# Kernel tuning notes

Measured on AMD Instinct MI355X. Metric: run time of the kernel, lower is better.

## Reference

```python
import jax, jax.numpy as jnp
import numpy as np

B, L, D, H, NB = 32, 200, 512, 8, 2
HD = D // H
EPS = 1e-8


def _ln(x, g, b):
    m = x.mean(-1, keepdims=True)
    v = ((x - m) ** 2).mean(-1, keepdims=True)
    return (x - m) / jnp.sqrt(v + EPS) * g + b


def setup_inputs() -> dict:
    key = jax.random.key(0)
    ks = jax.random.split(key, 12)
    w = lambda k, shape: (jax.random.normal(k, shape, jnp.float32) * 0.02)
    return {
        "x": jax.random.normal(ks[0], (B, L, D), jnp.float32),
        "timeline_mask": jnp.zeros((B, L), dtype=bool),  # True = padded
        "ln1_g": jnp.ones((NB, D), jnp.float32), "ln1_b": jnp.zeros((NB, D), jnp.float32),
        "Wq": w(ks[1], (NB, D, D)), "bq": jnp.zeros((NB, D), jnp.float32),
        "Wk": w(ks[2], (NB, D, D)), "bk": jnp.zeros((NB, D), jnp.float32),
        "Wv": w(ks[3], (NB, D, D)), "bv": jnp.zeros((NB, D), jnp.float32),
        "Wo": w(ks[4], (NB, D, D)), "bo": jnp.zeros((NB, D), jnp.float32),
        "ln2_g": jnp.ones((NB, D), jnp.float32), "ln2_b": jnp.zeros((NB, D), jnp.float32),
        "W1": w(ks[5], (NB, D, D)), "b1": jnp.zeros((NB, D), jnp.float32),
        "W2": w(ks[6], (NB, D, D)), "b2": jnp.zeros((NB, D), jnp.float32),
        "lnf_g": jnp.ones((D,), jnp.float32), "lnf_b": jnp.zeros((D,), jnp.float32),
    }


def reference(x, timeline_mask, ln1_g, ln1_b, Wq, bq, Wk, bk, Wv, bv, Wo, bo,
              ln2_g, ln2_b, W1, b1, W2, b2, lnf_g, lnf_b):
    valid = (~timeline_mask)[..., None].astype(x.dtype)  # [B,L,1]
    # causal additive bias [L,L]: 0 on/below diag, -inf above
    causal = jnp.where(jnp.tril(jnp.ones((L, L), dtype=bool)), 0.0, -jnp.inf).astype(x.dtype)
    scale = 1.0 / (HD ** 0.5)
    q = x * valid  # dropout = identity (eval)
    for i in range(NB):
        Qn = _ln(q, ln1_g[i], ln1_b[i])  # pre-attn LayerNorm (query side)
        qh = (Qn @ Wq[i] + bq[i]).reshape(B, L, H, HD)
        kh = (q @ Wk[i] + bk[i]).reshape(B, L, H, HD)
        vh = (q @ Wv[i] + bv[i]).reshape(B, L, H, HD)
        scores = jnp.einsum('bqhd,bkhd->bhqk', qh, kh) * scale + causal
        attn = jax.nn.softmax(scores, axis=-1)
        ctx = jnp.einsum('bhqk,bkhd->bqhd', attn, vh).reshape(B, L, D)
        q = ctx @ Wo[i] + bo[i] + Qn          # residual to normed Q (as in source)
        q = _ln(q, ln2_g[i], ln2_b[i])        # forward layernorm
        h = jax.nn.relu(q @ W1[i] + b1[i]) @ W2[i] + b2[i]  # 1x1 convs == per-token MLP
        q = (q + h) * valid                   # PWFF residual, then timeline mask
    return _ln(q, lnf_g, lnf_b)
```

## Files before the change

kernel.cpp:

```cpp
#include <hip/hip_runtime.h>

typedef unsigned short u16;
typedef __bf16 bfloat;
typedef bfloat bf16x8 __attribute__((ext_vector_type(8)));
typedef float f32x4 __attribute__((ext_vector_type(4)));
typedef u16 v8u16 __attribute__((ext_vector_type(8)));
typedef u16 v4u16 __attribute__((ext_vector_type(4)));

#define B_ 32
#define L_ 200
#define D_ 512
#define H_ 8
#define HD_ 64
#define M_ (B_*L_)

__device__ __forceinline__ float bf2f(u16 u) {
  union { float f; unsigned int i; } v; v.i = ((unsigned int)u) << 16; return v.f;
}
__device__ __forceinline__ u16 f2bf(float f) {
  union { float f; unsigned int i; } v; v.f = f;
  unsigned int i = v.i;
  return (u16)((i + 0x7FFFu + ((i >> 16) & 1u)) >> 16);
}

__device__ __forceinline__ void gload16(const void* g, void* l) {
  __builtin_amdgcn_global_load_lds(
      (const __attribute__((address_space(1))) void*)g,
      (__attribute__((address_space(3))) void*)l,
      16, 0, 0);
}

struct TPtrs { const float* s[12]; };

__global__ __launch_bounds__(256) void prep_kernel(
    const float* __restrict__ x, const unsigned char* __restrict__ mask,
    u16* __restrict__ qb, TPtrs tp, u16* __restrict__ dst)
{
  __shared__ float T[64][65];
  int bid = blockIdx.x;
  int t = threadIdx.x;
  if (bid < 1600) {
    size_t i = (size_t)bid * 256 + t;
    size_t base = i * 8;
    int tok = (int)(base >> 9);
    float valid = mask[tok] ? 0.f : 1.f;
    float4 v0 = *(const float4*)(x + base);
    float4 v1 = *(const float4*)(x + base + 4);
    v8u16 ob;
    ob[0]=f2bf(v0.x*valid); ob[1]=f2bf(v0.y*valid); ob[2]=f2bf(v0.z*valid); ob[3]=f2bf(v0.w*valid);
    ob[4]=f2bf(v1.x*valid); ob[5]=f2bf(v1.y*valid); ob[6]=f2bf(v1.z*valid); ob[7]=f2bf(v1.w*valid);
    *(v8u16*)(qb + base) = ob;
  } else {
    int wb   = bid - 1600;
    int mat  = wb >> 6;
    int tile = wb & 63;
    int tr = tile >> 3, tc = tile & 7;
    const float* src = tp.s[mat];
    #pragma unroll
    for (int i = 0; i < 4; i++) {
      int idx = t + i * 256;
      int row = idx >> 4, c4 = idx & 15;
      float4 v = *(const float4*)(src + (size_t)(tr * 64 + row) * 512 + tc * 64 + c4 * 4);
      T[row][c4 * 4 + 0] = v.x; T[row][c4 * 4 + 1] = v.y;
      T[row][c4 * 4 + 2] = v.z; T[row][c4 * 4 + 3] = v.w;
    }
    __syncthreads();
    u16* d = dst + (size_t)mat * 262144;
    #pragma unroll
    for (int i = 0; i < 2; i++) {
      int idx = t + i * 256;
      int row = idx >> 3, c8 = idx & 7;
      v8u16 v;
      #pragma unroll
      for (int j = 0; j < 8; j++) v[j] = f2bf(T[c8 * 8 + j][row]);
      *(v8u16*)(d + (size_t)(tc * 64 + row) * 512 + tr * 64 + c8 * 8) = v;
    }
  }
}

template<bool OUTF32>
__global__ __launch_bounds__(256) void ln_kernel(
    const u16* __restrict__ in, const float* __restrict__ g, const float* __restrict__ b,
    u16* __restrict__ outb, float* __restrict__ outf)
{
  int row  = blockIdx.x * 4 + (threadIdx.x >> 6);
  int lane = threadIdx.x & 63;
  size_t base = (size_t)row * 512 + lane * 8;
  v8u16 xv = *(const v8u16*)(in + base);
  float xs[8];
  #pragma unroll
  for (int j = 0; j < 8; j++) xs[j] = bf2f(xv[j]);
  float s = 0.f, q = 0.f;
  #pragma unroll
  for (int j = 0; j < 8; j++) { s += xs[j]; q += xs[j] * xs[j]; }
  #pragma unroll
  for (int off = 1; off < 64; off <<= 1) { s += __shfl_xor(s, off); q += __shfl_xor(q, off); }
  float mean = s * (1.f / 512.f);
  float var  = fmaxf(q * (1.f / 512.f) - mean * mean, 0.f);
  float rstd = rsqrtf(var + 1e-8f);
  float4 g0 = *(const float4*)(g + lane * 8);
  float4 g1 = *(const float4*)(g + lane * 8 + 4);
  float4 b0 = *(const float4*)(b + lane * 8);
  float4 b1 = *(const float4*)(b + lane * 8 + 4);
  float gv[8] = {g0.x,g0.y,g0.z,g0.w,g1.x,g1.y,g1.z,g1.w};
  float bv[8] = {b0.x,b0.y,b0.z,b0.w,b1.x,b1.y,b1.z,b1.w};
  if (OUTF32) {
    float of[8];
    #pragma unroll
    for (int j = 0; j < 8; j++) of[j] = (xs[j] - mean) * rstd * gv[j] + bv[j];
    *(float4*)(outf + base)     = make_float4(of[0], of[1], of[2], of[3]);
    *(float4*)(outf + base + 4) = make_float4(of[4], of[5], of[6], of[7]);
  } else {
    v8u16 ob;
    #pragma unroll
    for (int j = 0; j < 8; j++) ob[j] = f2bf((xs[j] - mean) * rstd * gv[j] + bv[j]);
    *(v8u16*)(outb + base) = ob;
  }
}

template<bool RELU, bool HAS_RES, bool MASK>
__device__ __forceinline__ void gemm_body(
    const u16* __restrict__ A, const u16* __restrict__ Wt, const float* __restrict__ bias,
    const u16* __restrict__ res, const unsigned char* __restrict__ mask,
    u16* __restrict__ outb, int m0, int n0, u16* As, u16* Bs)
{
  int tid = threadIdx.x, wid = tid >> 6, lane = tid & 63;
  int wr = wid >> 1, wc = wid & 1;
  int l15 = lane & 15, hi = lane >> 4;
  int sr8 = lane >> 3;
  int gsw = (lane & 7) ^ sr8;

  f32x4 acc[2][4] = {};

  for (int s = 0; s < 8; s++) {
    int kk = s * 64;
    #pragma unroll
    for (int i = 0; i < 2; i++) {
      int rbase = i * 32 + wid * 8;
      gload16(A + (size_t)(m0 + rbase + sr8) * 512 + kk + gsw * 8, (char*)As + rbase * 128);
    }
    #pragma unroll
    for (int j = 0; j < 4; j++) {
      int rbase = j * 32 + wid * 8;
      gload16(Wt + (size_t)(n0 + rbase + sr8) * 512 + kk + gsw * 8, (char*)Bs + rbase * 128);
    }
    __syncthreads();
    #pragma unroll
    for (int ksub = 0; ksub < 2; ksub++) {
      int ga = ksub * 4 + hi;
      bf16x8 af[2], bfr[4];
      #pragma unroll
      for (int mi = 0; mi < 2; mi++) {
        int ra = wr * 32 + mi * 16 + l15;
        af[mi] = *(const bf16x8*)(As + ra * 64 + ((ga ^ (ra & 7)) * 8));
      }
      #pragma unroll
      for (int ni = 0; ni < 4; ni++) {
        int rb = wc * 64 + ni * 16 + l15;
        bfr[ni] = *(const bf16x8*)(Bs + rb * 64 + ((ga ^ (rb & 7)) * 8));
      }
      #pragma unroll
      for (int mi = 0; mi < 2; mi++)
        #pragma unroll
        for (int ni = 0; ni < 4; ni++)
          acc[mi][ni] = __builtin_amdgcn_mfma_f32_16x16x32_bf16(af[mi], bfr[ni], acc[mi][ni], 0, 0, 0);
    }
    __syncthreads();
  }

  #pragma unroll
  for (int ni = 0; ni < 4; ni++) {
    int gc = n0 + wc * 64 + ni * 16 + l15;
    float bvv = bias[gc];
    #pragma unroll
    for (int mi = 0; mi < 2; mi++) {
      int grb = m0 + wr * 32 + mi * 16 + hi * 4;
      #pragma unroll
      for (int r = 0; r < 4; r++) {
        int gr = grb + r;
        float v = acc[mi][ni][r] + bvv;
        if (HAS_RES) v += bf2f(res[(size_t)gr * 512 + gc]);
        if (RELU) v = fmaxf(v, 0.f);
        if (MASK) v = mask[gr] ? 0.f : v;
        outb[(size_t)gr * 512 + gc] = f2bf(v);
      }
    }
  }
}

template<bool RELU, bool HAS_RES, bool MASK>
__global__ __launch_bounds__(256) void gemm_one(
    const u16* __restrict__ A, const u16* __restrict__ Wt, const float* __restrict__ bias,
    const u16* __restrict__ res, const unsigned char* __restrict__ mask,
    u16* __restrict__ outb)
{
  __shared__ u16 As[64 * 64];
  __shared__ u16 Bs[128 * 64];
  int bid = blockIdx.x;
  int m0 = (bid >> 2) * 64, n0 = (bid & 3) * 128;
  gemm_body<RELU, HAS_RES, MASK>(A, Wt, bias, res, mask, outb, m0, n0, As, Bs);
}

__global__ __launch_bounds__(256) void gemm_qkv(
    const u16* __restrict__ Aq, const u16* __restrict__ Akv,
    const u16* __restrict__ Wtq, const u16* __restrict__ Wtk, const u16* __restrict__ Wtv,
    const float* __restrict__ bq, const float* __restrict__ bk, const float* __restrict__ bv,
    u16* __restrict__ outq, u16* __restrict__ outk, u16* __restrict__ outv)
{
  __shared__ u16 As[64 * 64];
  __shared__ u16 Bs[128 * 64];
  int bid = blockIdx.x;
  int mat = bid / 400;
  int r = bid - mat * 400;
  int m0 = (r >> 2) * 64, n0 = (r & 3) * 128;
  const u16*   A    = (mat == 0) ? Aq  : Akv;
  const u16*   Wt   = (mat == 0) ? Wtq : ((mat == 1) ? Wtk : Wtv);
  const float* bias = (mat == 0) ? bq  : ((mat == 1) ? bk  : bv);
  u16*         outb = (mat == 0) ? outq : ((mat == 1) ? outk : outv);
  gemm_body<false, false, false>(A, Wt, bias, nullptr, nullptr, outb, m0, n0, As, Bs);
}

__global__ __launch_bounds__(256) void transposeV(const u16* __restrict__ Vh, u16* __restrict__ Vt) {
  int bh = blockIdx.x, b = bh >> 3, h = bh & 7;
  __shared__ u16 T[64 * 224];
  int tid = threadIdx.x;
  v8u16 z = {0,0,0,0,0,0,0,0};
  for (int idx = tid; idx < 64 * 224 / 8; idx += 256) *(v8u16*)(T + idx * 8) = z;
  __syncthreads();
  const u16* src = Vh + (size_t)(b * L_) * D_ + h * HD_;
  for (int idx = tid; idx < 200 * 8; idx += 256) {
    int l = idx >> 3, c = idx & 7;
    v8u16 v = *(const v8u16*)(src + (size_t)l * D_ + c * 8);
    #pragma unroll
    for (int j = 0; j < 8; j++) T[(c * 8 + j) * 224 + l] = v[j];
  }
  __syncthreads();
  u16* dst = Vt + (size_t)bh * 64 * 224;
  for (int idx = tid; idx < 64 * 224 / 8; idx += 256) *(v8u16*)(dst + idx * 8) = *(const v8u16*)(T + idx * 8);
}

__global__ __launch_bounds__(256) void attn_kernel(
    const u16* __restrict__ Qh, const u16* __restrict__ Kh,
    const u16* __restrict__ Vt, u16* __restrict__ ctx)
{
  __shared__ u16 Kl[208 * 64];
  __shared__ u16 Pl[4 * 16 * 224];
  int bh = blockIdx.x, b = bh >> 3, h = bh & 7;
  int tid = threadIdx.x;

  const u16* Kg = Kh + (size_t)(b * L_) * D_ + h * HD_;
  for (int idx = tid; idx < 208 * 8; idx += 256) {
    int row = idx >> 3, c = idx & 7;
    v8u16 v = {0,0,0,0,0,0,0,0};
    if (row < L_) v = *(const v8u16*)(Kg + (size_t)row * D_ + c * 8);
    *(v8u16*)(Kl + row * 64 + c * 8) = v;
  }
  __syncthreads();

  int wid = tid >> 6, lane = tid & 63;
  int l15 = lane & 15, hi = lane >> 4;
  u16* Pw = Pl + wid * 16 * 224;
  const u16* Vg = Vt + (size_t)bh * 64 * 224;
  {
    v4u16 z4 = {0,0,0,0};
    *(v4u16*)(Pw + l15 * 224 + 208 + hi * 4) = z4;
  }

  for (int t = wid; t < 13; t += 4) {
    int q0 = t * 16;
    int qrow = q0 + l15; if (qrow > L_ - 1) qrow = L_ - 1;
    const u16* Qg = Qh + (size_t)(b * L_ + qrow) * D_ + h * HD_ + hi * 8;
    bf16x8 aq0 = *(const bf16x8*)(Qg);
    bf16x8 aq1 = *(const bf16x8*)(Qg + 32);

    f32x4 sv[13];
    float m0[4];
    #pragma unroll
    for (int r = 0; r < 4; r++) m0[r] = -3.0e38f;

    #pragma unroll
    for (int kt = 0; kt < 13; kt++) {
      const u16* kp = Kl + (kt * 16 + l15) * 64 + hi * 8;
      bf16x8 bk0 = *(const bf16x8*)(kp);
      bf16x8 bk1 = *(const bf16x8*)(kp + 32);
      f32x4 a = {0.f, 0.f, 0.f, 0.f};
      a = __builtin_amdgcn_mfma_f32_16x16x32_bf16(aq0, bk0, a, 0, 0, 0);
      a = __builtin_amdgcn_mfma_f32_16x16x32_bf16(aq1, bk1, a, 0, 0, 0);
      #pragma unroll
      for (int r = 0; r < 4; r++) {
        int qr = q0 + hi * 4 + r;
        int kc = kt * 16 + l15;
        float val = (kc <= qr && qr < L_) ? a[r] * 0.125f : -3.0e38f;
        sv[kt][r] = val;
        m0[r] = fmaxf(m0[r], val);
      }
    }
    #pragma unroll
    for (int r = 0; r < 4; r++) {
      #pragma unroll
      for (int off = 1; off < 16; off <<= 1)
        m0[r] = fmaxf(m0[r], __shfl_xor(m0[r], off));
      if (m0[r] < -1e37f) m0[r] = 0.f;
    }
    float sum[4] = {0.f, 0.f, 0.f, 0.f};
    #pragma unroll
    for (int kt = 0; kt < 13; kt++) {
      #pragma unroll
      for (int r = 0; r < 4; r++) {
        float p = __expf(sv[kt][r] - m0[r]);
        sv[kt][r] = p;
        sum[r] += p;
      }
    }
    #pragma unroll
    for (int r = 0; r < 4; r++) {
      #pragma unroll
      for (int off = 1; off < 16; off <<= 1) sum[r] += __shfl_xor(sum[r], off);
    }
    float inv[4];
    #pragma unroll
    for (int r = 0; r < 4; r++) inv[r] = sum[r] > 0.f ? 1.f / sum[r] : 0.f;

    #pragma unroll
    for (int kt = 0; kt < 13; kt++) {
      #pragma unroll
      for (int r = 0; r < 4; r++)
        Pw[(hi * 4 + r) * 224 + kt * 16 + l15] = f2bf(sv[kt][r]);
    }
    asm volatile("" ::: "memory");

    #pragma unroll
    for (int nt = 0; nt < 4; nt++) {
      f32x4 a = {0.f, 0.f, 0.f, 0.f};
      #pragma unroll
      for (int ks = 0; ks < 7; ks++) {
        bf16x8 ap = *(const bf16x8*)(Pw + l15 * 224 + ks * 32 + hi * 8);
        bf16x8 bv = *(const bf16x8*)(Vg + (nt * 16 + l15) * 224 + ks * 32 + hi * 8);
        a = __builtin_amdgcn_mfma_f32_16x16x32_bf16(ap, bv, a, 0, 0, 0);
      }
      #pragma unroll
      for (int r = 0; r < 4; r++) {
        int qr = q0 + hi * 4 + r;
        if (qr < L_) ctx[(size_t)(b * L_ + qr) * D_ + h * HD_ + nt * 16 + l15] = f2bf(a[r] * inv[r]);
      }
    }
    asm volatile("" ::: "memory");
  }
}

extern "C" void kernel_launch(void* const* d_in, const int* in_sizes, int n_in,
                              void* d_out, int out_size, void* d_ws, size_t ws_size,
                              hipStream_t stream)
{
  (void)in_sizes; (void)n_in; (void)out_size; (void)ws_size;
  const float* x    = (const float*)d_in[0];
  const unsigned char* mask = (const unsigned char*)d_in[1];
  const float* ln1g = (const float*)d_in[2];
  const float* ln1b = (const float*)d_in[3];
  const float* Wq   = (const float*)d_in[4];
  const float* bq   = (const float*)d_in[5];
  const float* Wk   = (const float*)d_in[6];
  const float* bk   = (const float*)d_in[7];
  const float* Wv   = (const float*)d_in[8];
  const float* bv   = (const float*)d_in[9];
  const float* Wo   = (const float*)d_in[10];
  const float* bo   = (const float*)d_in[11];
  const float* ln2g = (const float*)d_in[12];
  const float* ln2b = (const float*)d_in[13];
  const float* W1   = (const float*)d_in[14];
  const float* b1   = (const float*)d_in[15];
  const float* W2   = (const float*)d_in[16];
  const float* b2   = (const float*)d_in[17];
  const float* lnfg = (const float*)d_in[18];
  const float* lnfb = (const float*)d_in[19];

  char* ws = (char*)d_ws;
  u16* Wt  = (u16*)(ws);
  u16* qb  = (u16*)(ws +  6291456);
  u16* Qn  = (u16*)(ws + 12845056);
  u16* qh  = (u16*)(ws + 19398656);
  u16* kh  = (u16*)(ws + 25952256);
  u16* vh  = (u16*)(ws + 32505856);
  u16* Vtb = (u16*)(ws + 39059456);

  TPtrs tp;
  tp.s[0] = Wq; tp.s[1] = Wq + 262144;
  tp.s[2] = Wk; tp.s[3] = Wk + 262144;
  tp.s[4] = Wv; tp.s[5] = Wv + 262144;
  tp.s[6] = Wo; tp.s[7] = Wo + 262144;
  tp.s[8] = W1; tp.s[9] = W1 + 262144;
  tp.s[10] = W2; tp.s[11] = W2 + 262144;

  prep_kernel<<<dim3(2368), dim3(256), 0, stream>>>(x, mask, qb, tp, Wt);

  for (int i = 0; i < 2; i++) {
    const u16* Wtq = Wt + (size_t)(0 + i) * 262144;
    const u16* Wtk = Wt + (size_t)(2 + i) * 262144;
    const u16* Wtv = Wt + (size_t)(4 + i) * 262144;
    const u16* Wto = Wt + (size_t)(6 + i) * 262144;
    const u16* Wt1 = Wt + (size_t)(8 + i) * 262144;
    const u16* Wt2 = Wt + (size_t)(10 + i) * 262144;

    ln_kernel<false><<<dim3(1600), dim3(256), 0, stream>>>(qb, ln1g + i * 512, ln1b + i * 512, Qn, nullptr);
    gemm_qkv<<<dim3(1200), dim3(256), 0, stream>>>(Qn, qb, Wtq, Wtk, Wtv,
                                                   bq + i * 512, bk + i * 512, bv + i * 512,
                                                   qh, kh, vh);
    transposeV<<<dim3(256), dim3(256), 0, stream>>>(vh, Vtb);
    attn_kernel<<<dim3(256), dim3(256), 0, stream>>>(qh, kh, Vtb, vh);
    gemm_one<false,true,false><<<dim3(400), dim3(256), 0, stream>>>(vh, Wto, bo + i * 512, Qn, nullptr, qb);
    ln_kernel<false><<<dim3(1600), dim3(256), 0, stream>>>(qb, ln2g + i * 512, ln2b + i * 512, Qn, nullptr);
    gemm_one<true,false,false><<<dim3(400), dim3(256), 0, stream>>>(Qn, Wt1, b1 + i * 512, nullptr, nullptr, qh);
    gemm_one<false,true,true><<<dim3(400), dim3(256), 0, stream>>>(qh, Wt2, b2 + i * 512, Qn, mask, qb);
  }
  ln_kernel<true><<<dim3(1600), dim3(256), 0, stream>>>(qb, lnfg, lnfb, nullptr, (float*)d_out);
}
```

Before: 211.2 us.

## Double-buffer GEMM k-loop, fuse V transpose into QKV epilogue, skip causal tiles

The GEMM core now prefetches the next k-slice into a second LDS buffer while computing on the current one, using explicit vmcnt waits and raw barriers. The QKV GEMM writes V directly in the transposed per-head layout, so the separate transposeV kernel and its round trip are removed. Attention skips QK^T, exp and PV work for key tiles above the causal diagonal. A risk: the padded columns of the transposed V buffer are no longer zeroed, so garbage there could leak into the last PV tile.

```diff
diff --git a/kernel.cpp b/kernel.cpp
--- a/kernel.cpp
+++ b/kernel.cpp
@@ -118,11 +118,9 @@
   }
 }
 
-template<bool RELU, bool HAS_RES, bool MASK>
-__device__ __forceinline__ void gemm_body(
-    const u16* __restrict__ A, const u16* __restrict__ Wt, const float* __restrict__ bias,
-    const u16* __restrict__ res, const unsigned char* __restrict__ mask,
-    u16* __restrict__ outb, int m0, int n0, u16* As, u16* Bs)
+__device__ __forceinline__ void gemm_core(
+    const u16* __restrict__ A, const u16* __restrict__ Wt,
+    int m0, int n0, u16* As, u16* Bs, f32x4 (&acc)[2][4])
 {
   int tid = threadIdx.x, wid = tid >> 6, lane = tid & 63;
   int wr = wid >> 1, wc = wid & 1;
@@ -130,21 +128,34 @@
   int sr8 = lane >> 3;
   int gsw = (lane & 7) ^ sr8;
 
-  f32x4 acc[2][4] = {};
-
+#define STAGE(buf, kk) do { \
+    _Pragma("unroll") \
+    for (int i_ = 0; i_ < 2; i_++) { \
+      int rb_ = i_ * 32 + wid * 8; \
+      gload16(A + (size_t)(m0 + rb_ + sr8) * 512 + (kk) + gsw * 8, \
+              (char*)As + (buf) * 8192 + rb_ * 128); \
+    } \
+    _Pragma("unroll") \
+    for (int j_ = 0; j_ < 4; j_++) { \
+      int rb_ = j_ * 32 + wid * 8; \
+      gload16(Wt + (size_t)(n0 + rb_ + sr8) * 512 + (kk) + gsw * 8, \
+              (char*)Bs + (buf) * 16384 + rb_ * 128); \
+    } } while (0)
+
+  STAGE(0, 0);
+  #pragma unroll
   for (int s = 0; s < 8; s++) {
-    int kk = s * 64;
-    #pragma unroll
-    for (int i = 0; i < 2; i++) {
-      int rbase = i * 32 + wid * 8;
-      gload16(A + (size_t)(m0 + rbase + sr8) * 512 + kk + gsw * 8, (char*)As + rbase * 128);
-    }
-    #pragma unroll
-    for (int j = 0; j < 4; j++) {
-      int rbase = j * 32 + wid * 8;
-      gload16(Wt + (size_t)(n0 + rbase + sr8) * 512 + kk + gsw * 8, (char*)Bs + rbase * 128);
-    }
-    __syncthreads();
+    int cur = s & 1;
+    if (s < 7) {
+      STAGE(cur ^ 1, (s + 1) * 64);
+      asm volatile("s_waitcnt vmcnt(6)" ::: "memory");
+    } else {
+      asm volatile("s_waitcnt vmcnt(0)" ::: "memory");
+    }
+    __builtin_amdgcn_s_barrier();
+    __builtin_amdgcn_sched_barrier(0);
+    const u16* Asb = As + cur * 4096;
+    const u16* Bsb = Bs + cur * 8192;
     #pragma unroll
     for (int ksub = 0; ksub < 2; ksub++) {
       int ga = ksub * 4 + hi;
@@ -152,12 +163,12 @@
       #pragma unroll
       for (int mi = 0; mi < 2; mi++) {
         int ra = wr * 32 + mi * 16 + l15;
-        af[mi] = *(const bf16x8*)(As + ra * 64 + ((ga ^ (ra & 7)) * 8));
+        af[mi] = *(const bf16x8*)(Asb + ra * 64 + ((ga ^ (ra & 7)) * 8));
       }
       #pragma unroll
       for (int ni = 0; ni < 4; ni++) {
         int rb = wc * 64 + ni * 16 + l15;
-        bfr[ni] = *(const bf16x8*)(Bs + rb * 64 + ((ga ^ (rb & 7)) * 8));
+        bfr[ni] = *(const bf16x8*)(Bsb + rb * 64 + ((ga ^ (rb & 7)) * 8));
       }
       #pragma unroll
       for (int mi = 0; mi < 2; mi++)
@@ -165,9 +176,28 @@
         for (int ni = 0; ni < 4; ni++)
           acc[mi][ni] = __builtin_amdgcn_mfma_f32_16x16x32_bf16(af[mi], bfr[ni], acc[mi][ni], 0, 0, 0);
     }
-    __syncthreads();
-  }
-
+    __builtin_amdgcn_sched_barrier(0);
+    __builtin_amdgcn_s_barrier();
+  }
+#undef STAGE
+}
+
+template<bool RELU, bool HAS_RES, bool MASK>
+__global__ __launch_bounds__(256) void gemm_one(
+    const u16* __restrict__ A, const u16* __restrict__ Wt, const float* __restrict__ bias,
+    const u16* __restrict__ res, const unsigned char* __restrict__ mask,
+    u16* __restrict__ outb)
+{
+  __shared__ u16 As[2 * 64 * 64];
+  __shared__ u16 Bs[2 * 128 * 64];
+  int bid = blockIdx.x;
+  int m0 = (bid >> 2) * 64, n0 = (bid & 3) * 128;
+  f32x4 acc[2][4] = {};
+  gemm_core(A, Wt, m0, n0, As, Bs, acc);
+
+  int tid = threadIdx.x, wid = tid >> 6, lane = tid & 63;
+  int wr = wid >> 1, wc = wid & 1;
+  int l15 = lane & 15, hi = lane >> 4;
   #pragma unroll
   for (int ni = 0; ni < 4; ni++) {
     int gc = n0 + wc * 64 + ni * 16 + l15;
@@ -188,55 +218,61 @@
   }
 }
 
-template<bool RELU, bool HAS_RES, bool MASK>
-__global__ __launch_bounds__(256) void gemm_one(
-    const u16* __restrict__ A, const u16* __restrict__ Wt, const float* __restrict__ bias,
-    const u16* __restrict__ res, const unsigned char* __restrict__ mask,
-    u16* __restrict__ outb)
-{
-  __shared__ u16 As[64 * 64];
-  __shared__ u16 Bs[128 * 64];
-  int bid = blockIdx.x;
-  int m0 = (bid >> 2) * 64, n0 = (bid & 3) * 128;
-  gemm_body<RELU, HAS_RES, MASK>(A, Wt, bias, res, mask, outb, m0, n0, As, Bs);
-}
-
 __global__ __launch_bounds__(256) void gemm_qkv(
     const u16* __restrict__ Aq, const u16* __restrict__ Akv,
     const u16* __restrict__ Wtq, const u16* __restrict__ Wtk, const u16* __restrict__ Wtv,
     const float* __restrict__ bq, const float* __restrict__ bk, const float* __restrict__ bv,
-    u16* __restrict__ outq, u16* __restrict__ outk, u16* __restrict__ outv)
-{
-  __shared__ u16 As[64 * 64];
-  __shared__ u16 Bs[128 * 64];
+    u16* __restrict__ outq, u16* __restrict__ outk, u16* __restrict__ outvt)
+{
+  __shared__ u16 As[2 * 64 * 64];
+  __shared__ u16 Bs[2 * 128 * 64];
   int bid = blockIdx.x;
   int mat = bid / 400;
-  int r = bid - mat * 400;
-  int m0 = (r >> 2) * 64, n0 = (r & 3) * 128;
+  int rr = bid - mat * 400;
+  int m0 = (rr >> 2) * 64, n0 = (rr & 3) * 128;
   const u16*   A    = (mat == 0) ? Aq  : Akv;
   const u16*   Wt   = (mat == 0) ? Wtq : ((mat == 1) ? Wtk : Wtv);
   const float* bias = (mat == 0) ? bq  : ((mat == 1) ? bk  : bv);
-  u16*         outb = (mat == 0) ? outq : ((mat == 1) ? outk : outv);
-  gemm_body<false, false, false>(A, Wt, bias, nullptr, nullptr, outb, m0, n0, As, Bs);
-}
-
-__global__ __launch_bounds__(256) void transposeV(const u16* __restrict__ Vh, u16* __restrict__ Vt) {
-  int bh = blockIdx.x, b = bh >> 3, h = bh & 7;
-  __shared__ u16 T[64 * 224];
-  int tid = threadIdx.x;
-  v8u16 z = {0,0,0,0,0,0,0,0};
-  for (int idx = tid; idx < 64 * 224 / 8; idx += 256) *(v8u16*)(T + idx * 8) = z;
-  __syncthreads();
-  const u16* src = Vh + (size_t)(b * L_) * D_ + h * HD_;
-  for (int idx = tid; idx < 200 * 8; idx += 256) {
-    int l = idx >> 3, c = idx & 7;
-    v8u16 v = *(const v8u16*)(src + (size_t)l * D_ + c * 8);
-    #pragma unroll
-    for (int j = 0; j < 8; j++) T[(c * 8 + j) * 224 + l] = v[j];
-  }
-  __syncthreads();
-  u16* dst = Vt + (size_t)bh * 64 * 224;
-  for (int idx = tid; idx < 64 * 224 / 8; idx += 256) *(v8u16*)(dst + idx * 8) = *(const v8u16*)(T + idx * 8);
+  f32x4 acc[2][4] = {};
+  gemm_core(A, Wt, m0, n0, As, Bs, acc);
+
+  int tid = threadIdx.x, wid = tid >> 6, lane = tid & 63;
+  int wr = wid >> 1, wc = wid & 1;
+  int l15 = lane & 15, hi = lane >> 4;
+  if (mat == 2) {
+    #pragma unroll
+    for (int ni = 0; ni < 4; ni++) {
+      int gc = n0 + wc * 64 + ni * 16 + l15;
+      float bvv = bias[gc];
+      int h = gc >> 6, hd = gc & 63;
+      #pragma unroll
+      for (int mi = 0; mi < 2; mi++) {
+        int grb = m0 + wr * 32 + mi * 16 + hi * 4;
+        #pragma unroll
+        for (int r = 0; r < 4; r++) {
+          int gr = grb + r;
+          int b = gr / 200, l = gr - b * 200;
+          outvt[((size_t)(b * 8 + h) * 64 + hd) * 224 + l] = f2bf(acc[mi][ni][r] + bvv);
+        }
+      }
+    }
+  } else {
+    u16* outb = (mat == 0) ? outq : outk;
+    #pragma unroll
+    for (int ni = 0; ni < 4; ni++) {
+      int gc = n0 + wc * 64 + ni * 16 + l15;
+      float bvv = bias[gc];
+      #pragma unroll
+      for (int mi = 0; mi < 2; mi++) {
+        int grb = m0 + wr * 32 + mi * 16 + hi * 4;
+        #pragma unroll
+        for (int r = 0; r < 4; r++) {
+          int gr = grb + r;
+          outb[(size_t)gr * 512 + gc] = f2bf(acc[mi][ni][r] + bvv);
+        }
+      }
+    }
+  }
 }
 
 __global__ __launch_bounds__(256) void attn_kernel(
@@ -280,19 +316,24 @@
 
     #pragma unroll
     for (int kt = 0; kt < 13; kt++) {
-      const u16* kp = Kl + (kt * 16 + l15) * 64 + hi * 8;
-      bf16x8 bk0 = *(const bf16x8*)(kp);
-      bf16x8 bk1 = *(const bf16x8*)(kp + 32);
-      f32x4 a = {0.f, 0.f, 0.f, 0.f};
-      a = __builtin_amdgcn_mfma_f32_16x16x32_bf16(aq0, bk0, a, 0, 0, 0);
-      a = __builtin_amdgcn_mfma_f32_16x16x32_bf16(aq1, bk1, a, 0, 0, 0);
-      #pragma unroll
-      for (int r = 0; r < 4; r++) {
-        int qr = q0 + hi * 4 + r;
-        int kc = kt * 16 + l15;
-        float val = (kc <= qr && qr < L_) ? a[r] * 0.125f : -3.0e38f;
-        sv[kt][r] = val;
-        m0[r] = fmaxf(m0[r], val);
+      if (kt <= t) {
+        const u16* kp = Kl + (kt * 16 + l15) * 64 + hi * 8;
+        bf16x8 bk0 = *(const bf16x8*)(kp);
+        bf16x8 bk1 = *(const bf16x8*)(kp + 32);
+        f32x4 a = {0.f, 0.f, 0.f, 0.f};
+        a = __builtin_amdgcn_mfma_f32_16x16x32_bf16(aq0, bk0, a, 0, 0, 0);
+        a = __builtin_amdgcn_mfma_f32_16x16x32_bf16(aq1, bk1, a, 0, 0, 0);
+        #pragma unroll
+        for (int r = 0; r < 4; r++) {
+          int qr = q0 + hi * 4 + r;
+          int kc = kt * 16 + l15;
+          float val = (kc <= qr && qr < L_) ? a[r] * 0.125f : -3.0e38f;
+          sv[kt][r] = val;
+          m0[r] = fmaxf(m0[r], val);
+        }
+      } else {
+        #pragma unroll
+        for (int r = 0; r < 4; r++) sv[kt][r] = -3.0e38f;
       }
     }
     #pragma unroll
@@ -305,11 +346,16 @@
     float sum[4] = {0.f, 0.f, 0.f, 0.f};
     #pragma unroll
     for (int kt = 0; kt < 13; kt++) {
-      #pragma unroll
-      for (int r = 0; r < 4; r++) {
-        float p = __expf(sv[kt][r] - m0[r]);
-        sv[kt][r] = p;
-        sum[r] += p;
+      if (kt <= t) {
+        #pragma unroll
+        for (int r = 0; r < 4; r++) {
+          float p = __expf(sv[kt][r] - m0[r]);
+          sv[kt][r] = p;
+          sum[r] += p;
+        }
+      } else {
+        #pragma unroll
+        for (int r = 0; r < 4; r++) sv[kt][r] = 0.f;
       }
     }
     #pragma unroll
@@ -329,14 +375,17 @@
     }
     asm volatile("" ::: "memory");
 
+    int ksmax = ((t + 1) * 16 + 31) >> 5;
     #pragma unroll
     for (int nt = 0; nt < 4; nt++) {
       f32x4 a = {0.f, 0.f, 0.f, 0.f};
       #pragma unroll
       for (int ks = 0; ks < 7; ks++) {
-        bf16x8 ap = *(const bf16x8*)(Pw + l15 * 224 + ks * 32 + hi * 8);
-        bf16x8 bv = *(const bf16x8*)(Vg + (nt * 16 + l15) * 224 + ks * 32 + hi * 8);
-        a = __builtin_amdgcn_mfma_f32_16x16x32_bf16(ap, bv, a, 0, 0, 0);
+        if (ks < ksmax) {
+          bf16x8 ap = *(const bf16x8*)(Pw + l15 * 224 + ks * 32 + hi * 8);
+          bf16x8 bv = *(const bf16x8*)(Vg + (nt * 16 + l15) * 224 + ks * 32 + hi * 8);
+          a = __builtin_amdgcn_mfma_f32_16x16x32_bf16(ap, bv, a, 0, 0, 0);
+        }
       }
       #pragma unroll
       for (int r = 0; r < 4; r++) {
@@ -404,8 +453,7 @@
     ln_kernel<false><<<dim3(1600), dim3(256), 0, stream>>>(qb, ln1g + i * 512, ln1b + i * 512, Qn, nullptr);
     gemm_qkv<<<dim3(1200), dim3(256), 0, stream>>>(Qn, qb, Wtq, Wtk, Wtv,
                                                    bq + i * 512, bk + i * 512, bv + i * 512,
-                                                   qh, kh, vh);
-    transposeV<<<dim3(256), dim3(256), 0, stream>>>(vh, Vtb);
+                                                   qh, kh, Vtb);
     attn_kernel<<<dim3(256), dim3(256), 0, stream>>>(qh, kh, Vtb, vh);
     gemm_one<false,true,false><<<dim3(400), dim3(256), 0, stream>>>(vh, Wto, bo + i * 512, Qn, nullptr, qb);
     ln_kernel<false><<<dim3(1600), dim3(256), 0, stream>>>(qb, ln2g + i * 512, ln2b + i * 512, Qn, nullptr);
```

New measurement: 213.8 us. No clear change (+1.2%).
